# Optimization experiments

Hardware: AMD Instinct MI355X
Metric: run time of the kernel (lower is better)

Reference implementation:

```python
import jax, jax.numpy as jnp
import numpy as np

NUM_EMB = 8192
EMB_DIM = 32
LATENT = 1024
COMMIT = 0.25
CB_COST = 1.0


def _l2norm(x, eps=1e-12):
    # matches torch F.normalize: x / max(||x||, eps)
    n = jnp.sqrt(jnp.sum(x * x, axis=-1, keepdims=True))
    return x / jnp.maximum(n, eps)


def setup_inputs() -> dict:
    key = jax.random.key(0)
    k = jax.random.split(key, 6)
    B = 32768
    s_in = 1.0 / np.sqrt(LATENT)
    s_out = 1.0 / np.sqrt(EMB_DIM)
    return {
        "z_e": jax.random.normal(k[0], (B, LATENT), jnp.float32),
        "in_w": jax.random.uniform(k[1], (EMB_DIM, LATENT), jnp.float32, -s_in, s_in),
        "in_b": jax.random.uniform(k[2], (EMB_DIM,), jnp.float32, -s_in, s_in),
        "out_w": jax.random.uniform(k[3], (LATENT, EMB_DIM), jnp.float32, -s_out, s_out),
        "out_b": jax.random.uniform(k[4], (LATENT,), jnp.float32, -s_out, s_out),
        "codebook": jax.random.normal(k[5], (NUM_EMB, EMB_DIM), jnp.float32),
    }


def reference(z_e, in_w, in_b, out_w, out_b, codebook):
    # in_proj: [B, LATENT] -> [B, EMB_DIM]
    ze = z_e @ in_w.T + in_b
    zn = _l2norm(ze)                      # [B, E]
    wn = _l2norm(codebook)                # [Z, E]
    # squared euclidean distance between normalized vectors
    dist = (jnp.sum(zn * zn, axis=1, keepdims=True)
            - 2.0 * (zn @ wn.T)
            + jnp.sum(wn * wn, axis=1))   # [B, Z]
    idx = jnp.argmin(dist, axis=1)        # [B]
    z_q = codebook[idx]                   # [B, E] (unnormalized codebook lookup)
    enc_loss = jnp.mean((ze - jax.lax.stop_gradient(z_q)) ** 2)
    cb_loss = jnp.mean((z_q - jax.lax.stop_gradient(ze)) ** 2)
    loss = CB_COST * cb_loss + COMMIT * enc_loss
    # straight-through estimator
    z_st = ze + jax.lax.stop_gradient(z_q - ze)
    out = z_st @ out_w.T + out_b          # [B, LATENT]
    return out, loss, enc_loss, cb_loss, idx, ze
```

## Files before the change

kernel.cpp:

```cpp
#include <hip/hip_runtime.h>
#include <hip/hip_bf16.h>

#define B_SZ    32768
#define LAT     1024
#define EMB     32
#define ZCB     8192
#define NSPL    8
#define RESC_CAP 32768
#define EPS_MARGIN 2e-4f

#define OFF_LOSS  ((size_t)B_SZ * LAT)
#define OFF_ENC   (OFF_LOSS + 1)
#define OFF_CB    (OFF_LOSS + 2)
#define OFF_IDX   (OFF_LOSS + 3)
#define OFF_ZE    (OFF_IDX + B_SZ)

#define WS_PZE    0
#define WS_PB1    0
#define WS_PB2    262144
#define WS_PIDXS  524288
#define WS_ZSTN   1048576
#define WS_ZEA    2097152
#define WS_ZNPK   3145728
#define WS_WPK    4194304
#define WS_IDXT   4456448
#define WS_CNT    4489216
#define WS_LIST   4489217
#define WS_LPART  4521985

typedef float  f32x4  __attribute__((ext_vector_type(4)));
typedef short  short8 __attribute__((ext_vector_type(8)));

__device__ __forceinline__ unsigned short f2bf(float x) {
    unsigned u = __float_as_uint(x);
    u += 0x7FFF + ((u >> 16) & 1);
    return (unsigned short)(u >> 16);
}
__device__ __forceinline__ float bf2f(unsigned short h) {
    return __uint_as_float(((unsigned)h) << 16);
}

__global__ __launch_bounds__(256) void knorm(const float* __restrict__ cb,
                                             short* __restrict__ wpk) {
    int e = threadIdx.x;
    int r = threadIdx.y;
    int row = blockIdx.x * 8 + r;
    float v = cb[row * EMB + e];
    float s = v * v;
    #pragma unroll
    for (int m = 16; m >= 1; m >>= 1) s += __shfl_xor(s, m, 64);
    float n = fmaxf(sqrtf(s), 1e-12f);
    float w = v / n;
    unsigned short h = f2bf(w);
    unsigned short l = f2bf(w - bf2f(h));
    wpk[row * 64 + e]      = (short)h;
    wpk[row * 64 + 32 + e] = (short)l;
}

#define KZB 64
#define KZS 68
__global__ __launch_bounds__(256) void kze2(const float* __restrict__ z_e,
                                            const float* __restrict__ in_w,
                                            float* __restrict__ pze) {
    __shared__ float zs[128 * KZS];
    __shared__ float wt[KZB * 32];
    int tid = threadIdx.x;
    size_t row0 = (size_t)blockIdx.x * 128;
    int ks = blockIdx.y;
    int rs = tid >> 2;
    int eg = tid & 3;
    int E  = eg * 8;

    float acc[2][8];
    #pragma unroll
    for (int i = 0; i < 2; ++i)
        #pragma unroll
        for (int j = 0; j < 8; ++j) acc[i][j] = 0.f;

    for (int c = 0; c < 512 / KZB; ++c) {
        int kb = ks * 512 + c * KZB;
        __syncthreads();
        #pragma unroll
        for (int i = 0; i < 8; ++i) {
            int t = tid + i * 256;
            int r = t >> 4, c4 = t & 15;
            float4 v = *(const float4*)(z_e + (row0 + r) * LAT + kb + c4 * 4);
            *(float4*)&zs[r * KZS + c4 * 4] = v;
        }
        #pragma unroll
        for (int i = 0; i < 2; ++i) {
            int t = tid + i * 256;
            int e = t >> 4, k4 = t & 15;
            float4 v = *(const float4*)(in_w + (size_t)e * LAT + kb + k4 * 4);
            float vv[4] = {v.x, v.y, v.z, v.w};
            #pragma unroll
            for (int j = 0; j < 4; ++j) {
                int k = k4 * 4 + j;
                wt[k * 32 + (e ^ ((k & 7) << 2))] = vv[j];
            }
        }
        __syncthreads();
        #pragma unroll 4
        for (int kq = 0; kq < KZB / 4; ++kq) {
            int k0 = kq * 4;
            float4 za = *(const float4*)&zs[rs * KZS + k0];
            float4 zb = *(const float4*)&zs[(rs + 64) * KZS + k0];
            float zav[4] = {za.x, za.y, za.z, za.w};
            float zbv[4] = {zb.x, zb.y, zb.z, zb.w};
            #pragma unroll
            for (int i = 0; i < 4; ++i) {
                int k = k0 + i;
                int sw = (k & 7) << 2;
                float4 w0 = *(const float4*)&wt[k * 32 + (E ^ sw)];
                float4 w1 = *(const float4*)&wt[k * 32 + ((E + 4) ^ sw)];
                float wa[8] = {w0.x, w0.y, w0.z, w0.w, w1.x, w1.y, w1.z, w1.w};
                #pragma unroll
                for (int j = 0; j < 8; ++j) {
                    acc[0][j] = fmaf(zav[i], wa[j], acc[0][j]);
                    acc[1][j] = fmaf(zbv[i], wa[j], acc[1][j]);
                }
            }
        }
    }
    size_t rb = ((size_t)ks * B_SZ + row0);
    float* p0 = pze + (rb + rs) * EMB + E;
    float* p1 = pze + (rb + rs + 64) * EMB + E;
    *(float4*)p0       = make_float4(acc[0][0], acc[0][1], acc[0][2], acc[0][3]);
    *(float4*)(p0 + 4) = make_float4(acc[0][4], acc[0][5], acc[0][6], acc[0][7]);
    *(float4*)p1       = make_float4(acc[1][0], acc[1][1], acc[1][2], acc[1][3]);
    *(float4*)(p1 + 4) = make_float4(acc[1][4], acc[1][5], acc[1][6], acc[1][7]);
}

__global__ __launch_bounds__(256) void kprep(const float* __restrict__ pze,
                                             const float* __restrict__ in_b,
                                             float* __restrict__ ze_out,
                                             float* __restrict__ ze_a,
                                             short* __restrict__ znpk) {
    int tid = threadIdx.x;
    size_t row = (size_t)blockIdx.x * 64 + (tid >> 2);
    int eg = tid & 3;
    const float* p0 = pze + row * 32 + eg * 8;
    const float* p1 = p0 + (size_t)B_SZ * 32;
    float4 a0 = *(const float4*)p0, a1 = *(const float4*)(p0 + 4);
    float4 b0 = *(const float4*)p1, b1 = *(const float4*)(p1 + 4);
    float4 c0 = *(const float4*)(in_b + eg * 8), c1 = *(const float4*)(in_b + eg * 8 + 4);
    float v[8];
    v[0] = a0.x + b0.x + c0.x; v[1] = a0.y + b0.y + c0.y;
    v[2] = a0.z + b0.z + c0.z; v[3] = a0.w + b0.w + c0.w;
    v[4] = a1.x + b1.x + c1.x; v[5] = a1.y + b1.y + c1.y;
    v[6] = a1.z + b1.z + c1.z; v[7] = a1.w + b1.w + c1.w;
    float nn = 0.f;
    #pragma unroll
    for (int i = 0; i < 8; ++i) nn = fmaf(v[i], v[i], nn);
    nn += __shfl_xor(nn, 1, 64);
    nn += __shfl_xor(nn, 2, 64);
    float n = fmaxf(sqrtf(nn), 1e-12f);

    *(float4*)(ze_a + row * 32 + eg * 8)     = make_float4(v[0], v[1], v[2], v[3]);
    *(float4*)(ze_a + row * 32 + eg * 8 + 4) = make_float4(v[4], v[5], v[6], v[7]);
    #pragma unroll
    for (int i = 0; i < 8; ++i) ze_out[row * 32 + eg * 8 + i] = v[i];

    short8 hv, lv;
    #pragma unroll
    for (int i = 0; i < 8; ++i) {
        float x = v[i] / n;
        unsigned short h = f2bf(x);
        unsigned short l = f2bf(x - bf2f(h));
        hv[i] = (short)h; lv[i] = (short)l;
    }
    *(short8*)(znpk + row * 64 + eg * 8)      = hv;
    *(short8*)(znpk + row * 64 + 32 + eg * 8) = lv;
}

__global__ __launch_bounds__(256) void kdistM(const short* __restrict__ znpk,
                                              const short* __restrict__ wpk,
                                              float* __restrict__ pb1,
                                              float* __restrict__ pb2,
                                              int*   __restrict__ pidxs) {
    int tid = threadIdx.x;
    int wave = tid >> 6, l = tid & 63;
    int l15 = l & 15, g = l >> 4;
    size_t rowbase = (size_t)blockIdx.x * 256 + wave * 64;
    int s = blockIdx.y;

    short8 zh[4], zl[4];
    #pragma unroll
    for (int rt = 0; rt < 4; ++rt) {
        const short8* p = (const short8*)(znpk + (rowbase + rt * 16 + l15) * 64 + g * 8);
        zh[rt] = p[0];
        zl[rt] = p[4];
    }
    f32x4 zero4 = {0.f, 0.f, 0.f, 0.f};
    float b1[16], b2[16]; int t1[16];
    #pragma unroll
    for (int i = 0; i < 16; ++i) { b1[i] = -1e30f; b2[i] = -1e30f; t1[i] = 0; }

    const short* wbase = wpk + ((size_t)s * 1024 + l15) * 64 + g * 8;
    for (int t = 0; t < 64; ++t) {
        const short8* wp = (const short8*)(wbase + (size_t)t * 1024);
        short8 bh = wp[0];
        short8 bl = wp[4];
        #pragma unroll
        for (int rt = 0; rt < 4; ++rt) {
            f32x4 acc = __builtin_amdgcn_mfma_f32_16x16x32_bf16(zh[rt], bh, zero4, 0, 0, 0);
            acc = __builtin_amdgcn_mfma_f32_16x16x32_bf16(zl[rt], bh, acc, 0, 0, 0);
            acc = __builtin_amdgcn_mfma_f32_16x16x32_bf16(zh[rt], bl, acc, 0, 0, 0);
            #pragma unroll
            for (int r = 0; r < 4; ++r) {
                int slot = rt * 4 + r;
                float d = acc[r];
                float mn = fminf(b1[slot], d);
                bool  c  = d > b1[slot];
                b1[slot] = fmaxf(b1[slot], d);
                b2[slot] = fmaxf(b2[slot], mn);
                t1[slot] = c ? t : t1[slot];
            }
        }
    }
    #pragma unroll
    for (int slot = 0; slot < 16; ++slot) {
        float B1 = b1[slot], B2 = b2[slot];
        int I = (t1[slot] << 4) | l15;
        #pragma unroll
        for (int m = 1; m <= 8; m <<= 1) {
            float ob  = __shfl_xor(B1, m, 64);
            float ob2 = __shfl_xor(B2, m, 64);
            int   oi  = __shfl_xor(I, m, 64);
            float mn = fminf(B1, ob);
            B2 = fmaxf(fmaxf(B2, ob2), mn);
            bool take = (ob > B1) || (ob == B1 && oi < I);
            B1 = take ? ob : B1;
            I  = take ? oi : I;
        }
        if (l15 == 0) {
            size_t row = rowbase + (size_t)(slot >> 2) * 16 + g * 4 + (slot & 3);
            pb1[(size_t)s * B_SZ + row] = B1;
            pb2[(size_t)s * B_SZ + row] = B2;
            pidxs[(size_t)s * B_SZ + row] = s * 1024 + I;
        }
    }
}

__global__ __launch_bounds__(256) void kmergeArg(const float* __restrict__ pb1,
                                                 const float* __restrict__ pb2,
                                                 const int* __restrict__ pidxs,
                                                 int* __restrict__ idxt,
                                                 int* __restrict__ cnt,
                                                 int* __restrict__ list) {
    int row = blockIdx.x * 256 + threadIdx.x;
    float best = pb1[row], second = pb2[row];
    int idx = pidxs[row];
    #pragma unroll
    for (int s = 1; s < NSPL; ++s) {
        float b  = pb1[(size_t)s * B_SZ + row];
        float sb = pb2[(size_t)s * B_SZ + row];
        int   i2 = pidxs[(size_t)s * B_SZ + row];
        float mn = fminf(best, b);
        second = fmaxf(fmaxf(second, sb), mn);
        if (b > best) { best = b; idx = i2; }
    }
    idxt[row] = idx;
    if (best - second < EPS_MARGIN) {
        int p = atomicAdd(cnt, 1);
        if (p < RESC_CAP) list[p] = row;
    }
}

__global__ __launch_bounds__(256) void krescore(const float* __restrict__ ze_a,
                                                const float* __restrict__ cb,
                                                int* __restrict__ idxt,
                                                const int* __restrict__ cnt,
                                                const int* __restrict__ list) {
    __shared__ float bvs[4];
    __shared__ int   bis[4];
    int tid = threadIdx.x;
    int wave = tid >> 6, l = tid & 63;
    int gl = l & 7;
    int gj = l >> 3;
    int n = *cnt; if (n > RESC_CAP) n = RESC_CAP;
    for (int ii = blockIdx.x; ii < n; ii += gridDim.x) {
        int row = list[ii];
        float4 z = *(const float4*)(ze_a + (size_t)row * 32 + gl * 4);
        float zz = fmaf(z.x, z.x, fmaf(z.y, z.y, fmaf(z.z, z.z, z.w * z.w)));
        zz += __shfl_xor(zz, 1, 64);
        zz += __shfl_xor(zz, 2, 64);
        zz += __shfl_xor(zz, 4, 64);
        float zinv = 1.f / fmaxf(sqrtf(zz), 1e-12f);
        z.x *= zinv; z.y *= zinv; z.z *= zinv; z.w *= zinv;

        float best = -1e30f; int bi = 0;
        int jbase = wave * 2048 + gj;
        for (int b = 0; b < 32; ++b) {
            float w2v[8], dtv[8];
            #pragma unroll
            for (int cc = 0; cc < 8; ++cc) {
                int j = jbase + (b * 8 + cc) * 8;
                float4 w = *(const float4*)(cb + (size_t)j * 32 + gl * 4);
                w2v[cc] = fmaf(w.x, w.x, fmaf(w.y, w.y, fmaf(w.z, w.z, w.w * w.w)));
                dtv[cc] = fmaf(z.x, w.x, fmaf(z.y, w.y, fmaf(z.z, w.z, z.w * w.w)));
            }
            #pragma unroll
            for (int cc = 0; cc < 8; ++cc) {
                w2v[cc] += __shfl_xor(w2v[cc], 1, 64);
                dtv[cc] += __shfl_xor(dtv[cc], 1, 64);
            }
            #pragma unroll
            for (int cc = 0; cc < 8; ++cc) {
                w2v[cc] += __shfl_xor(w2v[cc], 2, 64);
                dtv[cc] += __shfl_xor(dtv[cc], 2, 64);
            }
            #pragma unroll
            for (int cc = 0; cc < 8; ++cc) {
                w2v[cc] += __shfl_xor(w2v[cc], 4, 64);
                dtv[cc] += __shfl_xor(dtv[cc], 4, 64);
            }
            #pragma unroll
            for (int cc = 0; cc < 8; ++cc) {
                int j = jbase + (b * 8 + cc) * 8;
                float inv = 1.f / fmaxf(sqrtf(w2v[cc]), 1e-12f);
                float m = dtv[cc] * inv - 0.5f * (w2v[cc] * inv * inv);
                if (m > best || (m == best && j < bi)) { best = m; bi = j; }
            }
        }
        #pragma unroll
        for (int mk = 8; mk <= 32; mk <<= 1) {
            float ob = __shfl_xor(best, mk, 64);
            int   oi = __shfl_xor(bi, mk, 64);
            bool take = (ob > best) || (ob == best && oi < bi);
            best = take ? ob : best;
            bi   = take ? oi : bi;
        }
        if (l == 0) { bvs[wave] = best; bis[wave] = bi; }
        __syncthreads();
        if (tid == 0) {
            float B = bvs[0]; int I = bis[0];
            #pragma unroll
            for (int w2i = 1; w2i < 4; ++w2i) {
                float ob = bvs[w2i]; int oi = bis[w2i];
                if (ob > B || (ob == B && oi < I)) { B = ob; I = oi; }
            }
            idxt[row] = I;
        }
        __syncthreads();
    }
}

__global__ __launch_bounds__(256) void kfinal(const int* __restrict__ idxt,
                                              const float* __restrict__ ze,
                                              const float* __restrict__ cb,
                                              float* __restrict__ out_idx,
                                              float* __restrict__ zst,
                                              float* __restrict__ lpart) {
    int tid = threadIdx.x;
    int row = blockIdx.x * 256 + tid;
    int bidx = idxt[row];
    out_idx[row] = (float)bidx;

    const float4* zq4 = (const float4*)(cb + (size_t)bidx * EMB);
    const float4* ze4 = (const float4*)(ze + (size_t)row * EMB);
    float4* zs4 = (float4*)(zst + (size_t)row * EMB);
    float sq = 0.f;
    #pragma unroll
    for (int i = 0; i < 8; ++i) {
        float4 q = zq4[i], z = ze4[i];
        float dx = z.x - q.x, dy = z.y - q.y, dz = z.z - q.z, dw = z.w - q.w;
        sq += (dx * dx + dy * dy) + (dz * dz + dw * dw);
        float4 o;
        o.x = z.x + (q.x - z.x); o.y = z.y + (q.y - z.y);
        o.z = z.z + (q.z - z.z); o.w = z.w + (q.w - z.w);
        zs4[i] = o;
    }
    #pragma unroll
    for (int m = 1; m <= 32; m <<= 1) sq += __shfl_xor(sq, m, 64);
    __shared__ float red[4];
    if ((tid & 63) == 0) red[tid >> 6] = sq;
    __syncthreads();
    if (tid == 0) lpart[blockIdx.x] = (red[0] + red[1]) + (red[2] + red[3]);
}

__global__ void kloss(const float* __restrict__ lpart, float* __restrict__ dout) {
    float v = lpart[threadIdx.x];
    #pragma unroll
    for (int m = 1; m <= 32; m <<= 1) v += __shfl_xor(v, m, 64);
    __shared__ float tmp[2];
    if ((threadIdx.x & 63) == 0) tmp[threadIdx.x >> 6] = v;
    __syncthreads();
    if (threadIdx.x == 0) {
        float enc = (tmp[0] + tmp[1]) / (float)(B_SZ * EMB);
        dout[OFF_LOSS] = 1.0f * enc + 0.25f * enc;
        dout[OFF_ENC]  = enc;
        dout[OFF_CB]   = enc;
    }
}

__global__ __launch_bounds__(256) void kout(const float* __restrict__ zst,
                                            const float* __restrict__ out_w,
                                            const float* __restrict__ out_b,
                                            float* __restrict__ out) {
    __shared__ float zsh[128 * EMB];
    int tid = threadIdx.x;
    int col = blockIdx.x * 512 + tid * 2;
    size_t row0 = (size_t)blockIdx.y * 128;
    {
        const float4* src = (const float4*)(zst + row0 * EMB);
        float4* dst = (float4*)zsh;
        #pragma unroll
        for (int i = 0; i < 4; ++i) dst[tid + i * 256] = src[tid + i * 256];
    }
    float wa[32], wb[32];
    {
        const float4* wa4 = (const float4*)(out_w + (size_t)col * EMB);
        const float4* wb4 = (const float4*)(out_w + (size_t)(col + 1) * EMB);
        #pragma unroll
        for (int i = 0; i < 8; ++i) {
            float4 a = wa4[i]; wa[4*i]=a.x; wa[4*i+1]=a.y; wa[4*i+2]=a.z; wa[4*i+3]=a.w;
            float4 b = wb4[i]; wb[4*i]=b.x; wb[4*i+1]=b.y; wb[4*i+2]=b.z; wb[4*i+3]=b.w;
        }
    }
    float b0 = out_b[col], b1 = out_b[col + 1];
    __syncthreads();
    for (int rr = 0; rr < 128; ++rr) {
        const float4* zr4 = (const float4*)(zsh + rr * EMB);
        float a0 = b0, a1 = b1;
        #pragma unroll
        for (int q = 0; q < 8; ++q) {
            float4 z = zr4[q];
            a0 = fmaf(z.x, wa[4*q],   a0); a1 = fmaf(z.x, wb[4*q],   a1);
            a0 = fmaf(z.y, wa[4*q+1], a0); a1 = fmaf(z.y, wb[4*q+1], a1);
            a0 = fmaf(z.z, wa[4*q+2], a0); a1 = fmaf(z.z, wb[4*q+2], a1);
            a0 = fmaf(z.w, wa[4*q+3], a0); a1 = fmaf(z.w, wb[4*q+3], a1);
        }
        float2 o; o.x = a0; o.y = a1;
        *(float2*)(out + (row0 + rr) * LAT + col) = o;
    }
}

extern "C" void kernel_launch(void* const* d_in, const int* in_sizes, int n_in,
                              void* d_out, int out_size, void* d_ws, size_t ws_size,
                              hipStream_t stream) {
    const float* z_e   = (const float*)d_in[0];
    const float* in_w  = (const float*)d_in[1];
    const float* in_b  = (const float*)d_in[2];
    const float* out_w = (const float*)d_in[3];
    const float* out_b = (const float*)d_in[4];
    const float* cb    = (const float*)d_in[5];

    float* out = (float*)d_out;
    float* ws  = (float*)d_ws;
    float* pze   = ws + WS_PZE;
    float* pb1   = ws + WS_PB1;
    float* pb2   = ws + WS_PB2;
    int*   pidxs = (int*)(ws + WS_PIDXS);
    float* zst   = ws + WS_ZSTN;
    float* ze_a  = ws + WS_ZEA;
    short* znpk  = (short*)(ws + WS_ZNPK);
    short* wpk   = (short*)(ws + WS_WPK);
    int*   idxt  = (int*)(ws + WS_IDXT);
    int*   cnt   = (int*)(ws + WS_CNT);
    int*   list  = (int*)(ws + WS_LIST);
    float* lpart = ws + WS_LPART;

    hipMemsetAsync((void*)cnt, 0, sizeof(int), stream);
    knorm    <<<dim3(ZCB / 8), dim3(32, 8), 0, stream>>>(cb, wpk);
    kze2     <<<dim3(B_SZ / 128, 2), 256, 0, stream>>>(z_e, in_w, pze);
    kprep    <<<dim3(B_SZ / 64), 256, 0, stream>>>(pze, in_b, out + OFF_ZE, ze_a, znpk);
    kdistM   <<<dim3(B_SZ / 256, NSPL), 256, 0, stream>>>(znpk, wpk, pb1, pb2, pidxs);
    kmergeArg<<<dim3(B_SZ / 256), 256, 0, stream>>>(pb1, pb2, pidxs, idxt, cnt, list);
    krescore <<<dim3(512), 256, 0, stream>>>(ze_a, cb, idxt, cnt, list);
    kfinal   <<<dim3(B_SZ / 256), 256, 0, stream>>>(idxt, ze_a, cb, out + OFF_IDX, zst, lpart);
    kloss    <<<1, 128, 0, stream>>>(lpart, out);
    kout     <<<dim3(2, B_SZ / 128), 256, 0, stream>>>(zst, out_w, out_b, out);
}
```

Baseline: 277.9 us.

## Drop argmax index tracking from MFMA distance loop and recover it in a separate pass

The hot MFMA distance loop now keeps only the best and second-best scores per lane, not the tile index, which removes a compare and select per element. A new krecover kernel re-scores the 8 tiles of the winning lane column for each row in fp32 to recover the exact codebook index. The straight-through buffer is no longer written by kfinal; kout gathers ze and codebook rows directly into shared memory. This adds a full extra pass over all rows (8 codebook rows each) and a gather inside kout, in exchange for a lighter inner loop and one less intermediate buffer write.

```diff
diff --git a/kernel.cpp b/kernel.cpp
--- a/kernel.cpp
+++ b/kernel.cpp
@@ -18,8 +18,8 @@
 #define WS_PZE    0
 #define WS_PB1    0
 #define WS_PB2    262144
-#define WS_PIDXS  524288
-#define WS_ZSTN   1048576
+#define WS_PL15   524288
+#define WS_CAND   1048576
 #define WS_ZEA    2097152
 #define WS_ZNPK   3145728
 #define WS_WPK    4194304
@@ -177,7 +177,7 @@
                                               const short* __restrict__ wpk,
                                               float* __restrict__ pb1,
                                               float* __restrict__ pb2,
-                                              int*   __restrict__ pidxs) {
+                                              int*   __restrict__ pl15) {
     int tid = threadIdx.x;
     int wave = tid >> 6, l = tid & 63;
     int l15 = l & 15, g = l >> 4;
@@ -192,9 +192,9 @@
         zl[rt] = p[4];
     }
     f32x4 zero4 = {0.f, 0.f, 0.f, 0.f};
-    float b1[16], b2[16]; int t1[16];
-    #pragma unroll
-    for (int i = 0; i < 16; ++i) { b1[i] = -1e30f; b2[i] = -1e30f; t1[i] = 0; }
+    float bb1[16], bb2[16];
+    #pragma unroll
+    for (int i = 0; i < 16; ++i) { bb1[i] = -1e30f; bb2[i] = -1e30f; }
 
     const short* wbase = wpk + ((size_t)s * 1024 + l15) * 64 + g * 8;
     for (int t = 0; t < 64; ++t) {
@@ -210,60 +210,105 @@
             for (int r = 0; r < 4; ++r) {
                 int slot = rt * 4 + r;
                 float d = acc[r];
-                float mn = fminf(b1[slot], d);
-                bool  c  = d > b1[slot];
-                b1[slot] = fmaxf(b1[slot], d);
-                b2[slot] = fmaxf(b2[slot], mn);
-                t1[slot] = c ? t : t1[slot];
+                float mn = fminf(bb1[slot], d);
+                bb1[slot] = fmaxf(bb1[slot], d);
+                bb2[slot] = fmaxf(bb2[slot], mn);
             }
         }
     }
     #pragma unroll
     for (int slot = 0; slot < 16; ++slot) {
-        float B1 = b1[slot], B2 = b2[slot];
-        int I = (t1[slot] << 4) | l15;
+        float B1 = bb1[slot], B2 = bb2[slot];
+        int ID = l15;
         #pragma unroll
         for (int m = 1; m <= 8; m <<= 1) {
-            float ob  = __shfl_xor(B1, m, 64);
+            float ob1 = __shfl_xor(B1, m, 64);
             float ob2 = __shfl_xor(B2, m, 64);
-            int   oi  = __shfl_xor(I, m, 64);
-            float mn = fminf(B1, ob);
+            int   oid = __shfl_xor(ID, m, 64);
+            float mn = fminf(B1, ob1);
             B2 = fmaxf(fmaxf(B2, ob2), mn);
-            bool take = (ob > B1) || (ob == B1 && oi < I);
-            B1 = take ? ob : B1;
-            I  = take ? oi : I;
+            bool take = (ob1 > B1) || (ob1 == B1 && oid < ID);
+            B1 = take ? ob1 : B1;
+            ID = take ? oid : ID;
         }
         if (l15 == 0) {
             size_t row = rowbase + (size_t)(slot >> 2) * 16 + g * 4 + (slot & 3);
             pb1[(size_t)s * B_SZ + row] = B1;
             pb2[(size_t)s * B_SZ + row] = B2;
-            pidxs[(size_t)s * B_SZ + row] = s * 1024 + I;
+            pl15[(size_t)s * B_SZ + row] = ID;
         }
     }
 }
 
 __global__ __launch_bounds__(256) void kmergeArg(const float* __restrict__ pb1,
                                                  const float* __restrict__ pb2,
-                                                 const int* __restrict__ pidxs,
-                                                 int* __restrict__ idxt,
+                                                 const int* __restrict__ pl15,
+                                                 int* __restrict__ cand,
                                                  int* __restrict__ cnt,
                                                  int* __restrict__ list) {
     int row = blockIdx.x * 256 + threadIdx.x;
-    float best = pb1[row], second = pb2[row];
-    int idx = pidxs[row];
+    float best1 = pb1[row], best2 = pb2[row];
+    int c = pl15[row], wsn = 0;
     #pragma unroll
     for (int s = 1; s < NSPL; ++s) {
         float b  = pb1[(size_t)s * B_SZ + row];
         float sb = pb2[(size_t)s * B_SZ + row];
-        int   i2 = pidxs[(size_t)s * B_SZ + row];
-        float mn = fminf(best, b);
-        second = fmaxf(fmaxf(second, sb), mn);
-        if (b > best) { best = b; idx = i2; }
-    }
-    idxt[row] = idx;
-    if (best - second < EPS_MARGIN) {
+        int   li = pl15[(size_t)s * B_SZ + row];
+        float mn = fminf(best1, b);
+        best2 = fmaxf(fmaxf(best2, sb), mn);
+        if (b > best1) { best1 = b; c = li; wsn = s; }
+    }
+    cand[row] = wsn * 16 + c;
+    if (best1 - best2 < EPS_MARGIN) {
         int p = atomicAdd(cnt, 1);
         if (p < RESC_CAP) list[p] = row;
+    }
+}
+
+__global__ __launch_bounds__(256) void krecover(const float* __restrict__ ze_a,
+                                                const float* __restrict__ cb,
+                                                const int* __restrict__ cand,
+                                                int* __restrict__ idxt) {
+    int tid = threadIdx.x;
+    int l = tid & 63;
+    int gl = l & 7;
+    int gj = l >> 3;
+    int wid = (blockIdx.x * 256 + tid) >> 6;
+    for (int row = wid; row < B_SZ; row += 2048) {
+        int c = cand[row];
+        int s = c >> 4, lc = c & 15;
+        float4 z = *(const float4*)(ze_a + (size_t)row * 32 + gl * 4);
+        float zz = fmaf(z.x, z.x, fmaf(z.y, z.y, fmaf(z.z, z.z, z.w * z.w)));
+        zz += __shfl_xor(zz, 1, 64);
+        zz += __shfl_xor(zz, 2, 64);
+        zz += __shfl_xor(zz, 4, 64);
+        float zinv = 1.f / fmaxf(sqrtf(zz), 1e-12f);
+        z.x *= zinv; z.y *= zinv; z.z *= zinv; z.w *= zinv;
+
+        float best = -1e30f; int bi = 0;
+        #pragma unroll
+        for (int b = 0; b < 8; ++b) {
+            int t = b * 8 + gj;
+            int j = s * 1024 + t * 16 + lc;
+            float4 w = *(const float4*)(cb + (size_t)j * 32 + gl * 4);
+            float w2 = fmaf(w.x, w.x, fmaf(w.y, w.y, fmaf(w.z, w.z, w.w * w.w)));
+            float dt = fmaf(z.x, w.x, fmaf(z.y, w.y, fmaf(z.z, w.z, z.w * w.w)));
+            w2 += __shfl_xor(w2, 1, 64); dt += __shfl_xor(dt, 1, 64);
+            w2 += __shfl_xor(w2, 2, 64); dt += __shfl_xor(dt, 2, 64);
+            w2 += __shfl_xor(w2, 4, 64); dt += __shfl_xor(dt, 4, 64);
+            float inv = 1.f / fmaxf(sqrtf(w2), 1e-12f);
+            float m = dt * inv - 0.5f * (w2 * inv * inv);
+            if (m > best || (m == best && j < bi)) { best = m; bi = j; }
+        }
+        #pragma unroll
+        for (int mk = 8; mk <= 32; mk <<= 1) {
+            float ob = __shfl_xor(best, mk, 64);
+            int   oi = __shfl_xor(bi, mk, 64);
+            bool take = (ob > best) || (ob == best && oi < bi);
+            best = take ? ob : best;
+            bi   = take ? oi : bi;
+        }
+        if (l == 0) idxt[row] = bi;
     }
 }
 
@@ -350,7 +395,6 @@
                                               const float* __restrict__ ze,
                                               const float* __restrict__ cb,
                                               float* __restrict__ out_idx,
-                                              float* __restrict__ zst,
                                               float* __restrict__ lpart) {
     int tid = threadIdx.x;
     int row = blockIdx.x * 256 + tid;
@@ -359,17 +403,12 @@
 
     const float4* zq4 = (const float4*)(cb + (size_t)bidx * EMB);
     const float4* ze4 = (const float4*)(ze + (size_t)row * EMB);
-    float4* zs4 = (float4*)(zst + (size_t)row * EMB);
     float sq = 0.f;
     #pragma unroll
     for (int i = 0; i < 8; ++i) {
         float4 q = zq4[i], z = ze4[i];
         float dx = z.x - q.x, dy = z.y - q.y, dz = z.z - q.z, dw = z.w - q.w;
         sq += (dx * dx + dy * dy) + (dz * dz + dw * dw);
-        float4 o;
-        o.x = z.x + (q.x - z.x); o.y = z.y + (q.y - z.y);
-        o.z = z.z + (q.z - z.z); o.w = z.w + (q.w - z.w);
-        zs4[i] = o;
     }
     #pragma unroll
     for (int m = 1; m <= 32; m <<= 1) sq += __shfl_xor(sq, m, 64);
@@ -394,19 +433,29 @@
     }
 }
 
-__global__ __launch_bounds__(256) void kout(const float* __restrict__ zst,
+__global__ __launch_bounds__(256) void kout(const float* __restrict__ ze_a,
+                                            const int* __restrict__ idxt,
+                                            const float* __restrict__ cb,
                                             const float* __restrict__ out_w,
                                             const float* __restrict__ out_b,
                                             float* __restrict__ out) {
     __shared__ float zsh[128 * EMB];
+    __shared__ int ish[128];
     int tid = threadIdx.x;
     int col = blockIdx.x * 512 + tid * 2;
     size_t row0 = (size_t)blockIdx.y * 128;
-    {
-        const float4* src = (const float4*)(zst + row0 * EMB);
-        float4* dst = (float4*)zsh;
-        #pragma unroll
-        for (int i = 0; i < 4; ++i) dst[tid + i * 256] = src[tid + i * 256];
+    if (tid < 128) ish[tid] = idxt[row0 + tid];
+    __syncthreads();
+    #pragma unroll
+    for (int i = 0; i < 4; ++i) {
+        int flat = i * 256 + tid;
+        int r = flat >> 3, q = flat & 7;
+        float4 zv = *(const float4*)(ze_a + (row0 + r) * EMB + q * 4);
+        float4 qv = *(const float4*)(cb + (size_t)ish[r] * EMB + q * 4);
+        float4 o;
+        o.x = zv.x + (qv.x - zv.x); o.y = zv.y + (qv.y - zv.y);
+        o.z = zv.z + (qv.z - zv.z); o.w = zv.w + (qv.w - zv.w);
+        *(float4*)&zsh[r * EMB + q * 4] = o;
     }
     float wa[32], wb[32];
     {
@@ -451,8 +500,8 @@
     float* pze   = ws + WS_PZE;
     float* pb1   = ws + WS_PB1;
     float* pb2   = ws + WS_PB2;
-    int*   pidxs = (int*)(ws + WS_PIDXS);
-    float* zst   = ws + WS_ZSTN;
+    int*   pl15  = (int*)(ws + WS_PL15);
+    int*   cand  = (int*)(ws + WS_CAND);
     float* ze_a  = ws + WS_ZEA;
     short* znpk  = (short*)(ws + WS_ZNPK);
     short* wpk   = (short*)(ws + WS_WPK);
@@ -465,10 +514,11 @@
     knorm    <<<dim3(ZCB / 8), dim3(32, 8), 0, stream>>>(cb, wpk);
     kze2     <<<dim3(B_SZ / 128, 2), 256, 0, stream>>>(z_e, in_w, pze);
     kprep    <<<dim3(B_SZ / 64), 256, 0, stream>>>(pze, in_b, out + OFF_ZE, ze_a, znpk);
-    kdistM   <<<dim3(B_SZ / 256, NSPL), 256, 0, stream>>>(znpk, wpk, pb1, pb2, pidxs);
-    kmergeArg<<<dim3(B_SZ / 256), 256, 0, stream>>>(pb1, pb2, pidxs, idxt, cnt, list);
+    kdistM   <<<dim3(B_SZ / 256, NSPL), 256, 0, stream>>>(znpk, wpk, pb1, pb2, pl15);
+    kmergeArg<<<dim3(B_SZ / 256), 256, 0, stream>>>(pb1, pb2, pl15, cand, cnt, list);
+    krecover <<<dim3(512), 256, 0, stream>>>(ze_a, cb, cand, idxt);
     krescore <<<dim3(512), 256, 0, stream>>>(ze_a, cb, idxt, cnt, list);
-    kfinal   <<<dim3(B_SZ / 256), 256, 0, stream>>>(idxt, ze_a, cb, out + OFF_IDX, zst, lpart);
+    kfinal   <<<dim3(B_SZ / 256), 256, 0, stream>>>(idxt, ze_a, cb, out + OFF_IDX, lpart);
     kloss    <<<1, 128, 0, stream>>>(lpart, out);
-    kout     <<<dim3(2, B_SZ / 128), 256, 0, stream>>>(zst, out_w, out_b, out);
-}
+    kout     <<<dim3(2, B_SZ / 128), 256, 0, stream>>>(ze_a, idxt, cb, out_w, out_b, out);
+}
```

After: 318.2 us. +14.5%, slower.
